# Performance work log

Measured on AMD Instinct MI355X. Metric: run time of the kernel, lower is better.

Reference implementation:

```python
import jax, jax.numpy as jnp
import numpy as np

D_MODEL = 1024
EXPAND = 2
D_INNER = EXPAND * D_MODEL          # 2048
HEADDIM = 64
NHEADS = D_INNER // HEADDIM         # 32
D_STATE = 128
NGROUPS = 1
D_CONV = 4
CONV_DIM = D_INNER + 2 * NGROUPS * D_STATE   # 2304
D_IN_PROJ = 2 * D_INNER + 2 * NGROUPS * D_STATE + NHEADS  # 4384
EPS = 1e-5


def setup_inputs() -> dict:
    key = jax.random.key(0)
    ks = jax.random.split(key, 12)
    x = jax.random.normal(ks[0], (2, 2048, D_MODEL), dtype=jnp.float32)
    in_proj_w = jax.random.normal(ks[1], (D_IN_PROJ, D_MODEL), dtype=jnp.float32) * 0.02
    conv_w = jax.random.normal(ks[2], (CONV_DIM, D_CONV), dtype=jnp.float32) * 0.2
    conv_b = jax.random.normal(ks[3], (CONV_DIM,), dtype=jnp.float32) * 0.02
    # dt_bias from inverse-softplus of dt ~ U(1e-3, 0.1)
    dt = jnp.exp(jax.random.uniform(ks[4], (NHEADS,)) * (np.log(0.1) - np.log(1e-3)) + np.log(1e-3))
    dt_bias = dt + jnp.log(-jnp.expm1(-dt))
    A_log = jnp.log(jax.random.uniform(ks[5], (NHEADS,), minval=1.0, maxval=16.0))
    D_skip = jnp.ones((NHEADS,), dtype=jnp.float32)
    norm_w = jnp.ones((D_INNER,), dtype=jnp.float32)
    out_w = jax.random.normal(ks[6], (D_MODEL, D_INNER), dtype=jnp.float32) * 0.02
    ln_g = jnp.ones((D_MODEL,), dtype=jnp.float32)
    ln_b = jnp.zeros((D_MODEL,), dtype=jnp.float32)
    return {"x": x, "in_proj_w": in_proj_w, "conv_w": conv_w, "conv_b": conv_b,
            "dt_bias": dt_bias, "A_log": A_log, "D_skip": D_skip, "norm_w": norm_w,
            "out_w": out_w, "ln_g": ln_g, "ln_b": ln_b}


def _depthwise_causal_conv(x, w, b):
    # x: (B, L, C); w: (C, K); causal depthwise conv (torch Conv1d groups=C, padding=K-1, truncated)
    K = w.shape[1]
    y = jax.lax.conv_general_dilated(
        x.transpose(0, 2, 1), w[:, None, :], (1,), [(K - 1, 0)],
        feature_group_count=w.shape[0], dimension_numbers=("NCH", "OIH", "NCH"))
    return y.transpose(0, 2, 1) + b


def _ssd_scan(xh, dt, A, Bm, Cm):
    # xh: (B,L,H,P), dt: (B,L,H), A: (H,), Bm/Cm: (B,L,N)  (ngroups=1)
    dA = jnp.exp(dt * A)  # (B,L,H)

    def step(h, inp):
        dA_t, dt_t, x_t, B_t, C_t = inp
        h = dA_t[..., None, None] * h + jnp.einsum("bh,bhp,bn->bhpn", dt_t, x_t, B_t)
        y = jnp.einsum("bhpn,bn->bhp", h, C_t)
        return h, y

    Bsz, L, H, P = xh.shape
    N = Bm.shape[-1]
    h0 = jnp.zeros((Bsz, H, P, N), dtype=xh.dtype)
    inputs = (dA.transpose(1, 0, 2), dt.transpose(1, 0, 2),
              xh.transpose(1, 0, 2, 3), Bm.transpose(1, 0, 2), Cm.transpose(1, 0, 2))
    _, ys = jax.lax.scan(step, h0, inputs)  # ys: (L,B,H,P)
    return ys.transpose(1, 0, 2, 3)


def reference(x, in_proj_w, conv_w, conv_b, dt_bias, A_log, D_skip, norm_w, out_w, ln_g, ln_b):
    B, L, D = x.shape
    residual = x  # D is a multiple of 8 -> pad branch is a no-op

    zxbcdt = jnp.einsum("bld,ed->ble", x, in_proj_w)  # (B,L,D_IN_PROJ)
    z = zxbcdt[..., :D_INNER]
    xBC = zxbcdt[..., D_INNER:D_INNER + CONV_DIM]
    dt = jax.nn.softplus(zxbcdt[..., D_INNER + CONV_DIM:] + dt_bias)  # (B,L,H)

    xBC = jax.nn.silu(_depthwise_causal_conv(xBC, conv_w, conv_b))
    xh = xBC[..., :D_INNER].reshape(B, L, NHEADS, HEADDIM)
    Bm = xBC[..., D_INNER:D_INNER + D_STATE]
    Cm = xBC[..., D_INNER + D_STATE:]

    A = -jnp.exp(A_log)  # (H,)
    y = _ssd_scan(xh, dt, A, Bm, Cm)          # (B,L,H,P)
    y = y + xh * D_skip[None, None, :, None]  # D skip connection
    y = y.reshape(B, L, D_INNER)

    # gated RMSNorm: normalize y * silu(z)
    y = y * jax.nn.silu(z)
    y = y * jax.lax.rsqrt(jnp.mean(y * y, axis=-1, keepdims=True) + EPS) * norm_w

    out = jnp.einsum("ble,de->bld", y, out_w)  # (B,L,D)

    # block LayerNorm + residual (dropout p=0 -> identity)
    mu = jnp.mean(out, axis=-1, keepdims=True)
    var = jnp.mean(jnp.square(out - mu), axis=-1, keepdims=True)
    out = (out - mu) * jax.lax.rsqrt(var + EPS) * ln_g + ln_b
    return out + residual
```

## Files before the change

### kernel.cpp

```cpp
#include <hip/hip_runtime.h>
#include <math.h>

#define D_MODEL   1024
#define D_INNER   2048
#define HEADDIM   64
#define NHEADS    32
#define D_STATE   128
#define D_CONV    4
#define CONV_DIM  2304
#define D_IN_PROJ 4384
#define NPAD      4480
#define LSEQ      2048
#define BATCH     2
#define NROWS     4096
#define NC        32

typedef __attribute__((ext_vector_type(8))) short short8_t;
typedef __attribute__((ext_vector_type(4))) float f32x4;

#define MFMA16(a, b, c) __builtin_amdgcn_mfma_f32_16x16x32_bf16(a, b, c, 0, 0, 0)

#define GLDS(g, l) __builtin_amdgcn_global_load_lds( \
    (const __attribute__((address_space(1))) unsigned int*)(g), \
    (__attribute__((address_space(3))) unsigned int*)(l), 16, 0, 0)

__device__ __forceinline__ unsigned short f2bf(float f) {
  union { float f; unsigned int u; } v; v.f = f;
  unsigned int u = v.u + 0x7FFFu + ((v.u >> 16) & 1u);
  return (unsigned short)(u >> 16);
}
__device__ __forceinline__ float bf2f(unsigned short h) {
  union { unsigned int u; float f; } v; v.u = ((unsigned int)h) << 16;
  return v.f;
}

__device__ __forceinline__ short8_t lds_frag(const unsigned short* base, int row,
                                             int col, int rowlen) {
  int off = (row * rowlen + col) * 2;
  off ^= (row & 7) << 4;
  return *reinterpret_cast<const short8_t*>(
      reinterpret_cast<const char*>(base) + off);
}
__device__ __forceinline__ void lds_w32(unsigned short* base, int row, int col,
                                        int rowlen, unsigned int val) {
  int off = (row * rowlen + col) * 2;
  off ^= (row & 7) << 4;
  *reinterpret_cast<unsigned int*>(reinterpret_cast<char*>(base) + off) = val;
}
__device__ __forceinline__ void lds_w16(unsigned short* base, int row, int col,
                                        int rowlen, unsigned short val) {
  int off = (row * rowlen + col) * 2;
  off ^= (row & 7) << 4;
  *reinterpret_cast<unsigned short*>(reinterpret_cast<char*>(base) + off) = val;
}
__device__ __forceinline__ unsigned short lds_r16(const unsigned short* base,
                                                  int row, int col, int rowlen) {
  int off = (row * rowlen + col) * 2;
  off ^= (row & 7) << 4;
  return *reinterpret_cast<const unsigned short*>(
      reinterpret_cast<const char*>(base) + off);
}

__global__ __launch_bounds__(256) void gemm_bf16(
    const unsigned short* __restrict__ A, const unsigned short* __restrict__ B,
    float* __restrict__ C, int N, int K) {
  __shared__ unsigned short sA[128 * 64];
  __shared__ unsigned short sB[128 * 64];
  const int tid = threadIdx.x;
  const int row0 = blockIdx.y * 128;
  const int col0 = blockIdx.x * 128;
  const int l  = tid & 63;
  const int la = l & 15;
  const int lk = (l >> 4) * 8;
  const int w  = tid >> 6;
  const int wr = (w >> 1) * 64;
  const int wc = (w & 1) * 64;

  f32x4 acc[4][4];
  #pragma unroll
  for (int i = 0; i < 4; ++i)
    #pragma unroll
    for (int j = 0; j < 4; ++j) acc[i][j] = (f32x4){0.f, 0.f, 0.f, 0.f};

  for (int k0 = 0; k0 < K; k0 += 64) {
    __syncthreads();
    #pragma unroll
    for (int i = 0; i < 4; ++i) {
      int s = i * 256 + tid;
      int r = s >> 3;
      int j = s & 7;
      int jc = j ^ (r & 7);
      GLDS(&A[(size_t)(row0 + r) * K + k0 + jc * 8], &sA[s * 8]);
      GLDS(&B[(size_t)(col0 + r) * K + k0 + jc * 8], &sB[s * 8]);
    }
    __syncthreads();

    #pragma unroll
    for (int kk = 0; kk < 2; ++kk) {
      short8_t af[4], bfr[4];
      #pragma unroll
      for (int mi = 0; mi < 4; ++mi)
        af[mi] = lds_frag(sA, wr + mi * 16 + la, kk * 32 + lk, 64);
      #pragma unroll
      for (int ni = 0; ni < 4; ++ni)
        bfr[ni] = lds_frag(sB, wc + ni * 16 + la, kk * 32 + lk, 64);
      #pragma unroll
      for (int mi = 0; mi < 4; ++mi)
        #pragma unroll
        for (int ni = 0; ni < 4; ++ni)
          acc[mi][ni] = MFMA16(af[mi], bfr[ni], acc[mi][ni]);
    }
  }

  #pragma unroll
  for (int mi = 0; mi < 4; ++mi)
    #pragma unroll
    for (int ni = 0; ni < 4; ++ni)
      #pragma unroll
      for (int r = 0; r < 4; ++r) {
        int gm = row0 + wr + mi * 16 + (l >> 4) * 4 + r;
        int gn = col0 + wc + ni * 16 + la;
        if (gn < N) C[(size_t)gm * N + gn] = acc[mi][ni][r];
      }
}

__global__ __launch_bounds__(256) void cvt_bf16_kernel(
    const float* __restrict__ src, unsigned short* __restrict__ dst) {
  long i = (long)blockIdx.x * 256 + threadIdx.x;
  float4 a = *reinterpret_cast<const float4*>(&src[i * 8]);
  float4 b = *reinterpret_cast<const float4*>(&src[i * 8 + 4]);
  short8_t o;
  o[0] = (short)f2bf(a.x); o[1] = (short)f2bf(a.y);
  o[2] = (short)f2bf(a.z); o[3] = (short)f2bf(a.w);
  o[4] = (short)f2bf(b.x); o[5] = (short)f2bf(b.y);
  o[6] = (short)f2bf(b.z); o[7] = (short)f2bf(b.w);
  *reinterpret_cast<short8_t*>(&dst[i * 8]) = o;
}

__global__ __launch_bounds__(256) void cvt_w_kernel(
    const float* __restrict__ w, unsigned short* __restrict__ wbf) {
  long i = (long)blockIdx.x * 256 + threadIdx.x;
  int row = (int)(i >> 7);
  int c8  = (int)(i & 127) << 3;
  short8_t o = {0, 0, 0, 0, 0, 0, 0, 0};
  if (row < D_IN_PROJ) {
    float4 a = *reinterpret_cast<const float4*>(&w[(size_t)row * D_MODEL + c8]);
    float4 b = *reinterpret_cast<const float4*>(&w[(size_t)row * D_MODEL + c8 + 4]);
    o[0] = (short)f2bf(a.x); o[1] = (short)f2bf(a.y);
    o[2] = (short)f2bf(a.z); o[3] = (short)f2bf(a.w);
    o[4] = (short)f2bf(b.x); o[5] = (short)f2bf(b.y);
    o[6] = (short)f2bf(b.z); o[7] = (short)f2bf(b.w);
  }
  *reinterpret_cast<short8_t*>(&wbf[(size_t)row * D_MODEL + c8]) = o;
}

__global__ __launch_bounds__(256) void conv_silu_kernel(
    const float* __restrict__ zxbcdt, const float* __restrict__ conv_w,
    const float* __restrict__ conv_b, float* __restrict__ xconv) {
  const int c = blockIdx.x * 256 + threadIdx.x;
  const int l = blockIdx.y;
  const int b = blockIdx.z;
  const float* src = zxbcdt + ((size_t)b * LSEQ) * D_IN_PROJ + D_INNER + c;
  float w0 = conv_w[c * 4 + 0], w1 = conv_w[c * 4 + 1];
  float w2 = conv_w[c * 4 + 2], w3 = conv_w[c * 4 + 3];
  float acc = conv_b[c];
  if (l >= 3) acc = fmaf(w0, src[(size_t)(l - 3) * D_IN_PROJ], acc);
  if (l >= 2) acc = fmaf(w1, src[(size_t)(l - 2) * D_IN_PROJ], acc);
  if (l >= 1) acc = fmaf(w2, src[(size_t)(l - 1) * D_IN_PROJ], acc);
  acc = fmaf(w3, src[(size_t)l * D_IN_PROJ], acc);
  float s = acc / (1.f + expf(-acc));
  xconv[((size_t)b * LSEQ + l) * CONV_DIM + c] = s;
}

__global__ __launch_bounds__(256) void dt_kernel(
    const float* __restrict__ zxbcdt, const float* __restrict__ dt_bias,
    float* __restrict__ dt_out) {
  int idx = blockIdx.x * 256 + threadIdx.x;
  int h = idx & 31;
  int row = idx >> 5;
  float x = zxbcdt[(size_t)row * D_IN_PROJ + (D_INNER + CONV_DIM) + h] + dt_bias[h];
  float dt = (x > 20.f) ? x : log1pf(expf(x));
  dt_out[idx] = dt;
}

__global__ __launch_bounds__(256) void cumsum_kernel(
    const float* __restrict__ dt_s, const float* __restrict__ A_log,
    float* __restrict__ cumL) {
  int u = blockIdx.x * 4 + (threadIdx.x >> 6);
  int lane = threadIdx.x & 63;
  int h = u & 31;
  int bc = u >> 5;
  int row = bc * 64 + lane;
  float A = -expf(A_log[h]);
  float a = dt_s[(size_t)row * NHEADS + h] * A;
  #pragma unroll
  for (int off = 1; off < 64; off <<= 1) {
    float v = __shfl_up(a, off);
    if (lane >= off) a += v;
  }
  cumL[(size_t)u * 64 + lane] = a;
}

__global__ __launch_bounds__(256) void chunkstate_kernel(
    const float* __restrict__ xconv, const float* __restrict__ dt_s,
    const float* __restrict__ cumL, unsigned short* __restrict__ S) {
  const int bi = blockIdx.x;
  const int h  = bi & 31;
  const int bc = bi >> 5;
  const int row0 = bc * 64;
  const int tid = threadIdx.x;

  __shared__ unsigned short sBT[128 * 64];
  __shared__ unsigned short sXT[64 * 64];
  __shared__ float sw[64];

  if (tid < 64) {
    float L   = cumL[(size_t)bi * 64 + tid];
    float L63 = cumL[(size_t)bi * 64 + 63];
    sw[tid] = dt_s[(size_t)(row0 + tid) * NHEADS + h] * expf(L63 - L);
  }
  __syncthreads();

  #pragma unroll
  for (int i = 0; i < 16; ++i) {
    int idx = tid + i * 256;
    int s = idx >> 6, n2 = idx & 63;
    float2 v = *reinterpret_cast<const float2*>(
        &xconv[(size_t)(row0 + s) * CONV_DIM + D_INNER + n2 * 2]);
    lds_w16(sBT, n2 * 2 + 0, s, 64, f2bf(v.x));
    lds_w16(sBT, n2 * 2 + 1, s, 64, f2bf(v.y));
  }
  #pragma unroll
  for (int i = 0; i < 16; ++i) {
    int idx = tid + i * 256;
    int s = idx >> 6, p = idx & 63;
    float xv = xconv[(size_t)(row0 + s) * CONV_DIM + h * HEADDIM + p];
    lds_w16(sXT, p, s, 64, f2bf(xv * sw[s]));
  }
  __syncthreads();

  const int w  = tid >> 6;
  const int l  = tid & 63;
  const int la = l & 15;
  const int lk = (l >> 4) * 8;

  f32x4 acc[8];
  #pragma unroll
  for (int i = 0; i < 8; ++i) acc[i] = (f32x4){0.f, 0.f, 0.f, 0.f};

  #pragma unroll
  for (int ks = 0; ks < 2; ++ks) {
    short8_t a = lds_frag(sXT, 16 * w + la, ks * 32 + lk, 64);
    #pragma unroll
    for (int ni = 0; ni < 8; ++ni) {
      short8_t b = lds_frag(sBT, ni * 16 + la, ks * 32 + lk, 64);
      acc[ni] = MFMA16(a, b, acc[ni]);
    }
  }

  unsigned short* dst = S + (size_t)bi * (HEADDIM * D_STATE);
  #pragma unroll
  for (int ni = 0; ni < 8; ++ni)
    #pragma unroll
    for (int r = 0; r < 4; ++r) {
      int p = 16 * w + (l >> 4) * 4 + r;
      int n = ni * 16 + la;
      dst[p * D_STATE + n] = f2bf(acc[ni][r]);
    }
}

__global__ __launch_bounds__(256) void hscan_kernel(
    unsigned short* __restrict__ S, const float* __restrict__ cumL) {
  const int g  = blockIdx.x;
  const int bh = g >> 5;
  const int b  = bh >> 5;
  const int h  = bh & 31;
  const int e  = (g & 31) * 256 + threadIdx.x;

  float H = 0.f;
  #pragma unroll 4
  for (int c = 0; c < NC; ++c) {
    size_t u = (size_t)((b * NC + c) * NHEADS + h);
    float dA = expf(cumL[u * 64 + 63]);
    unsigned short sv = S[u * (HEADDIM * D_STATE) + e];
    S[u * (HEADDIM * D_STATE) + e] = f2bf(H);
    H = dA * H + bf2f(sv);
  }
}

__global__ __launch_bounds__(256) void chunk_kernel(
    const float* __restrict__ xconv, const float* __restrict__ dt_s,
    const float* __restrict__ cumL, const unsigned short* __restrict__ Hprev,
    const float* __restrict__ D_skip, unsigned short* __restrict__ y) {
  const int bi = blockIdx.x;
  const int h  = bi & 31;
  const int bc = bi >> 5;
  const int row0 = bc * 64;
  const int tid = threadIdx.x;

  __shared__ unsigned short sC[64 * 128];
  __shared__ unsigned short sB[64 * 128];
  __shared__ unsigned short sXT[64 * 64];
  __shared__ unsigned short sP[64 * 64];
  __shared__ float sL[64], sdt[64], seL[64];

  if (tid < 64) {
    float L = cumL[(size_t)bi * 64 + tid];
    sL[tid]  = L;
    seL[tid] = expf(L);
    sdt[tid] = dt_s[(size_t)(row0 + tid) * NHEADS + h];
  }

  #pragma unroll
  for (int i = 0; i < 16; ++i) {
    int idx = tid + i * 256;
    int r = idx >> 6, q = idx & 63;
    float4 v = *reinterpret_cast<const float4*>(
        &xconv[(size_t)(row0 + r) * CONV_DIM + D_INNER + q * 4]);
    unsigned int u0 = (unsigned int)f2bf(v.x) | ((unsigned int)f2bf(v.y) << 16);
    unsigned int u1 = (unsigned int)f2bf(v.z) | ((unsigned int)f2bf(v.w) << 16);
    if (q < 32) {
      lds_w32(sB, r, q * 4 + 0, 128, u0);
      lds_w32(sB, r, q * 4 + 2, 128, u1);
    } else {
      lds_w32(sC, r, (q - 32) * 4 + 0, 128, u0);
      lds_w32(sC, r, (q - 32) * 4 + 2, 128, u1);
    }
  }
  #pragma unroll
  for (int i = 0; i < 16; ++i) {
    int idx = tid + i * 256;
    int s = idx >> 6, p = idx & 63;
    float xv = xconv[(size_t)(row0 + s) * CONV_DIM + h * HEADDIM + p];
    lds_w16(sXT, p, s, 64, f2bf(xv));
  }
  __syncthreads();

  const int w  = tid >> 6;
  const int l  = tid & 63;
  const int la = l & 15;
  const int lk = (l >> 4) * 8;
  const int t0 = 16 * w;

  f32x4 g[4];
  #pragma unroll
  for (int i = 0; i < 4; ++i) g[i] = (f32x4){0.f, 0.f, 0.f, 0.f};
  #pragma unroll
  for (int ks = 0; ks < 4; ++ks) {
    short8_t a = lds_frag(sC, t0 + la, ks * 32 + lk, 128);
    #pragma unroll
    for (int si = 0; si < 4; ++si) {
      short8_t b = lds_frag(sB, si * 16 + la, ks * 32 + lk, 128);
      g[si] = MFMA16(a, b, g[si]);
    }
  }
  #pragma unroll
  for (int si = 0; si < 4; ++si)
    #pragma unroll
    for (int r = 0; r < 4; ++r) {
      int t = t0 + (l >> 4) * 4 + r;
      int s = si * 16 + la;
      float m = 0.f;
      if (s <= t) m = expf(sL[t] - sL[s]) * sdt[s] * g[si][r];
      lds_w16(sP, t, s, 64, f2bf(m));
    }
  __syncthreads();

  f32x4 o[4];
  #pragma unroll
  for (int i = 0; i < 4; ++i) o[i] = (f32x4){0.f, 0.f, 0.f, 0.f};

  const unsigned short* hb = Hprev + (size_t)bi * (HEADDIM * D_STATE);
  #pragma unroll
  for (int ks = 0; ks < 4; ++ks) {
    short8_t a = lds_frag(sC, t0 + la, ks * 32 + lk, 128);
    #pragma unroll
    for (int si = 0; si < 4; ++si) {
      int p = si * 16 + la;
      short8_t b = *reinterpret_cast<const short8_t*>(
          &hb[p * D_STATE + ks * 32 + lk]);
      o[si] = MFMA16(a, b, o[si]);
    }
  }
  #pragma unroll
  for (int si = 0; si < 4; ++si)
    #pragma unroll
    for (int r = 0; r < 4; ++r) {
      int t = t0 + (l >> 4) * 4 + r;
      o[si][r] *= seL[t];
    }
  #pragma unroll
  for (int ks = 0; ks < 2; ++ks) {
    short8_t a = lds_frag(sP, t0 + la, ks * 32 + lk, 64);
    #pragma unroll
    for (int si = 0; si < 4; ++si) {
      short8_t b = lds_frag(sXT, si * 16 + la, ks * 32 + lk, 64);
      o[si] = MFMA16(a, b, o[si]);
    }
  }
  const float Dh = D_skip[h];
  #pragma unroll
  for (int si = 0; si < 4; ++si)
    #pragma unroll
    for (int r = 0; r < 4; ++r) {
      int t = t0 + (l >> 4) * 4 + r;
      int p = si * 16 + la;
      float xv = bf2f(lds_r16(sXT, p, t, 64));
      y[(size_t)(row0 + t) * D_INNER + h * HEADDIM + p] = f2bf(o[si][r] + Dh * xv);
    }
}

__global__ __launch_bounds__(256) void gate_rms_kernel(
    unsigned short* __restrict__ y, const float* __restrict__ zxbcdt,
    const float* __restrict__ norm_w) {
  const int row = blockIdx.x;
  const int tid = threadIdx.x;
  float v[8];
  float acc = 0.f;
  #pragma unroll
  for (int i = 0; i < 8; ++i) {
    int d = i * 256 + tid;
    float ys = bf2f(y[(size_t)row * D_INNER + d]);
    float z  = zxbcdt[(size_t)row * D_IN_PROJ + d];
    float gz = z / (1.f + expf(-z));
    float val = ys * gz;
    v[i] = val;
    acc = fmaf(val, val, acc);
  }
  #pragma unroll
  for (int off = 32; off; off >>= 1) acc += __shfl_xor(acc, off);
  __shared__ float wsum[4];
  if ((tid & 63) == 0) wsum[tid >> 6] = acc;
  __syncthreads();
  float total = wsum[0] + wsum[1] + wsum[2] + wsum[3];
  float scale = rsqrtf(total / (float)D_INNER + 1e-5f);
  #pragma unroll
  for (int i = 0; i < 8; ++i) {
    int d = i * 256 + tid;
    y[(size_t)row * D_INNER + d] = f2bf(v[i] * scale * norm_w[d]);
  }
}

__global__ __launch_bounds__(256) void ln_kernel(
    const float* __restrict__ o, const float* __restrict__ x,
    const float* __restrict__ lng, const float* __restrict__ lnb,
    float* __restrict__ out) {
  const int row = blockIdx.x;
  const int tid = threadIdx.x;
  float v[4];
  float s = 0.f, s2 = 0.f;
  #pragma unroll
  for (int i = 0; i < 4; ++i) {
    int d = i * 256 + tid;
    float t = o[(size_t)row * D_MODEL + d];
    v[i] = t;
    s += t;
    s2 = fmaf(t, t, s2);
  }
  #pragma unroll
  for (int off = 32; off; off >>= 1) {
    s  += __shfl_xor(s, off);
    s2 += __shfl_xor(s2, off);
  }
  __shared__ float sa[4], sb[4];
  if ((tid & 63) == 0) { sa[tid >> 6] = s; sb[tid >> 6] = s2; }
  __syncthreads();
  s  = sa[0] + sa[1] + sa[2] + sa[3];
  s2 = sb[0] + sb[1] + sb[2] + sb[3];
  float mu  = s / (float)D_MODEL;
  float var = s2 / (float)D_MODEL - mu * mu;
  float inv = rsqrtf(var + 1e-5f);
  #pragma unroll
  for (int i = 0; i < 4; ++i) {
    int d = i * 256 + tid;
    out[(size_t)row * D_MODEL + d] =
        (v[i] - mu) * inv * lng[d] + lnb[d] + x[(size_t)row * D_MODEL + d];
  }
}

extern "C" void kernel_launch(void* const* d_in, const int* in_sizes, int n_in,
                              void* d_out, int out_size, void* d_ws, size_t ws_size,
                              hipStream_t stream) {
  const float* x         = (const float*)d_in[0];
  const float* in_proj_w = (const float*)d_in[1];
  const float* conv_w    = (const float*)d_in[2];
  const float* conv_b    = (const float*)d_in[3];
  const float* dt_bias   = (const float*)d_in[4];
  const float* A_log     = (const float*)d_in[5];
  const float* D_skip    = (const float*)d_in[6];
  const float* norm_w    = (const float*)d_in[7];
  const float* out_w     = (const float*)d_in[8];
  const float* ln_g      = (const float*)d_in[9];
  const float* ln_b      = (const float*)d_in[10];
  float* out = (float*)d_out;

  float* ws      = (float*)d_ws;
  float* zxbcdt  = ws;
  float* xconv   = zxbcdt + (size_t)NROWS * D_IN_PROJ;
  float* dt_s    = xconv + (size_t)NROWS * CONV_DIM;
  float* cumL    = dt_s + (size_t)NROWS * NHEADS;
  unsigned short* schp = (unsigned short*)(cumL + (size_t)BATCH * NC * NHEADS * 64);
  unsigned short* ybuf = schp + (size_t)BATCH * NC * NHEADS * HEADDIM * D_STATE;
  unsigned short* xbf  = ybuf + (size_t)NROWS * D_INNER;
  unsigned short* wbf  = xbf + (size_t)NROWS * D_MODEL;
  unsigned short* owbf = wbf + (size_t)NPAD * D_MODEL;
  float* outpre  = zxbcdt;

  cvt_bf16_kernel<<<dim3(NROWS * D_MODEL / 8 / 256), dim3(256), 0, stream>>>(
      x, xbf);
  cvt_w_kernel<<<dim3(NPAD * 128 / 256), dim3(256), 0, stream>>>(
      in_proj_w, wbf);
  cvt_bf16_kernel<<<dim3(D_MODEL * D_INNER / 8 / 256), dim3(256), 0, stream>>>(
      out_w, owbf);

  gemm_bf16<<<dim3(NPAD / 128, NROWS / 128), dim3(256), 0, stream>>>(
      xbf, wbf, zxbcdt, D_IN_PROJ, D_MODEL);

  conv_silu_kernel<<<dim3(CONV_DIM / 256, LSEQ, BATCH), dim3(256), 0, stream>>>(
      zxbcdt, conv_w, conv_b, xconv);

  dt_kernel<<<dim3(NROWS * NHEADS / 256), dim3(256), 0, stream>>>(
      zxbcdt, dt_bias, dt_s);

  cumsum_kernel<<<dim3(BATCH * NC * NHEADS / 4), dim3(256), 0, stream>>>(
      dt_s, A_log, cumL);

  chunkstate_kernel<<<dim3(BATCH * NC * NHEADS), dim3(256), 0, stream>>>(
      xconv, dt_s, cumL, schp);

  hscan_kernel<<<dim3(BATCH * NHEADS * 32), dim3(256), 0, stream>>>(
      schp, cumL);

  chunk_kernel<<<dim3(BATCH * NC * NHEADS), dim3(256), 0, stream>>>(
      xconv, dt_s, cumL, schp, D_skip, ybuf);

  gate_rms_kernel<<<dim3(NROWS), dim3(256), 0, stream>>>(
      ybuf, zxbcdt, norm_w);

  gemm_bf16<<<dim3(D_MODEL / 128, NROWS / 128), dim3(256), 0, stream>>>(
      ybuf, owbf, outpre, D_MODEL, D_INNER);

  ln_kernel<<<dim3(NROWS), dim3(256), 0, stream>>>(
      outpre, x, ln_g, ln_b, out);
}
```

Measured before the change: 351.9 us.

## Store in_proj output and conv activations in bf16, swizzle GEMM block order

The in_proj GEMM now writes its output as bf16, plus a separate fp32 buffer for the dt columns. The conv output is also kept in bf16, which roughly halves intermediate traffic for the conv, chunk, chunkstate and gate kernels. The conv kernel processes 128 timesteps per thread with a sliding window instead of one per block. Gate RMS uses vectorized 16-byte loads and stores. GEMM blocks are remapped with an XCD-style swizzle for L2 locality. The extra bf16 rounding of z, x, B and C adds precision loss, and the output alias now reuses the bf16 region as an fp32 outpre buffer.

```diff
diff --git a/kernel.cpp b/kernel.cpp
--- a/kernel.cpp
+++ b/kernel.cpp
@@ -61,14 +61,19 @@
       reinterpret_cast<const char*>(base) + off);
 }
 
+template <int MODE>
 __global__ __launch_bounds__(256) void gemm_bf16(
     const unsigned short* __restrict__ A, const unsigned short* __restrict__ B,
-    float* __restrict__ C, int N, int K) {
+    void* __restrict__ Cout, float* __restrict__ dtraw, int N, int K) {
   __shared__ unsigned short sA[128 * 64];
   __shared__ unsigned short sB[128 * 64];
   const int tid = threadIdx.x;
-  const int row0 = blockIdx.y * 128;
-  const int col0 = blockIdx.x * 128;
+  const int lin = blockIdx.y * gridDim.x + blockIdx.x;
+  const int cpx = (gridDim.x * gridDim.y) >> 3;
+  const int swz = (lin & 7) * cpx + (lin >> 3);
+  const int row0 = (swz / gridDim.x) * 128;
+  const int col0 = (swz % gridDim.x) * 128;
+
   const int l  = tid & 63;
   const int la = l & 15;
   const int lk = (l >> 4) * 8;
@@ -120,7 +125,14 @@
       for (int r = 0; r < 4; ++r) {
         int gm = row0 + wr + mi * 16 + (l >> 4) * 4 + r;
         int gn = col0 + wc + ni * 16 + la;
-        if (gn < N) C[(size_t)gm * N + gn] = acc[mi][ni][r];
+        if (gn < N) {
+          if constexpr (MODE == 0) {
+            ((float*)Cout)[(size_t)gm * N + gn] = acc[mi][ni][r];
+          } else {
+            ((unsigned short*)Cout)[(size_t)gm * N + gn] = f2bf(acc[mi][ni][r]);
+            if (gn >= N - 32) dtraw[(size_t)gm * 32 + (gn - (N - 32))] = acc[mi][ni][r];
+          }
+        }
       }
 }
 
@@ -155,30 +167,35 @@
 }
 
 __global__ __launch_bounds__(256) void conv_silu_kernel(
-    const float* __restrict__ zxbcdt, const float* __restrict__ conv_w,
-    const float* __restrict__ conv_b, float* __restrict__ xconv) {
-  const int c = blockIdx.x * 256 + threadIdx.x;
-  const int l = blockIdx.y;
-  const int b = blockIdx.z;
-  const float* src = zxbcdt + ((size_t)b * LSEQ) * D_IN_PROJ + D_INNER + c;
-  float w0 = conv_w[c * 4 + 0], w1 = conv_w[c * 4 + 1];
-  float w2 = conv_w[c * 4 + 2], w3 = conv_w[c * 4 + 3];
-  float acc = conv_b[c];
-  if (l >= 3) acc = fmaf(w0, src[(size_t)(l - 3) * D_IN_PROJ], acc);
-  if (l >= 2) acc = fmaf(w1, src[(size_t)(l - 2) * D_IN_PROJ], acc);
-  if (l >= 1) acc = fmaf(w2, src[(size_t)(l - 1) * D_IN_PROJ], acc);
-  acc = fmaf(w3, src[(size_t)l * D_IN_PROJ], acc);
-  float s = acc / (1.f + expf(-acc));
-  xconv[((size_t)b * LSEQ + l) * CONV_DIM + c] = s;
+    const unsigned short* __restrict__ zxb, const float* __restrict__ conv_w,
+    const float* __restrict__ conv_b, unsigned short* __restrict__ xconv) {
+  const int c  = blockIdx.x * 256 + threadIdx.x;
+  const int l0 = blockIdx.y * 128;
+  const int b  = blockIdx.z;
+  const unsigned short* src = zxb + ((size_t)b * LSEQ) * D_IN_PROJ + D_INNER + c;
+  const float w0 = conv_w[c * 4 + 0], w1 = conv_w[c * 4 + 1];
+  const float w2 = conv_w[c * 4 + 2], w3 = conv_w[c * 4 + 3];
+  const float bia = conv_b[c];
+  float x0 = (l0 >= 3) ? bf2f(src[(size_t)(l0 - 3) * D_IN_PROJ]) : 0.f;
+  float x1 = (l0 >= 2) ? bf2f(src[(size_t)(l0 - 2) * D_IN_PROJ]) : 0.f;
+  float x2 = (l0 >= 1) ? bf2f(src[(size_t)(l0 - 1) * D_IN_PROJ]) : 0.f;
+  unsigned short* dst = xconv + ((size_t)(b * LSEQ + l0)) * CONV_DIM + c;
+  #pragma unroll 4
+  for (int i = 0; i < 128; ++i) {
+    float x3 = bf2f(src[(size_t)(l0 + i) * D_IN_PROJ]);
+    float acc = fmaf(w3, x3, fmaf(w2, x2, fmaf(w1, x1, fmaf(w0, x0, bia))));
+    float s = acc / (1.f + expf(-acc));
+    dst[(size_t)i * CONV_DIM] = f2bf(s);
+    x0 = x1; x1 = x2; x2 = x3;
+  }
 }
 
 __global__ __launch_bounds__(256) void dt_kernel(
-    const float* __restrict__ zxbcdt, const float* __restrict__ dt_bias,
+    const float* __restrict__ dtraw, const float* __restrict__ dt_bias,
     float* __restrict__ dt_out) {
   int idx = blockIdx.x * 256 + threadIdx.x;
   int h = idx & 31;
-  int row = idx >> 5;
-  float x = zxbcdt[(size_t)row * D_IN_PROJ + (D_INNER + CONV_DIM) + h] + dt_bias[h];
+  float x = dtraw[idx] + dt_bias[h];
   float dt = (x > 20.f) ? x : log1pf(expf(x));
   dt_out[idx] = dt;
 }
@@ -202,7 +219,7 @@
 }
 
 __global__ __launch_bounds__(256) void chunkstate_kernel(
-    const float* __restrict__ xconv, const float* __restrict__ dt_s,
+    const unsigned short* __restrict__ xconv, const float* __restrict__ dt_s,
     const float* __restrict__ cumL, unsigned short* __restrict__ S) {
   const int bi = blockIdx.x;
   const int h  = bi & 31;
@@ -225,16 +242,16 @@
   for (int i = 0; i < 16; ++i) {
     int idx = tid + i * 256;
     int s = idx >> 6, n2 = idx & 63;
-    float2 v = *reinterpret_cast<const float2*>(
+    unsigned int v = *reinterpret_cast<const unsigned int*>(
         &xconv[(size_t)(row0 + s) * CONV_DIM + D_INNER + n2 * 2]);
-    lds_w16(sBT, n2 * 2 + 0, s, 64, f2bf(v.x));
-    lds_w16(sBT, n2 * 2 + 1, s, 64, f2bf(v.y));
+    lds_w16(sBT, n2 * 2 + 0, s, 64, (unsigned short)v);
+    lds_w16(sBT, n2 * 2 + 1, s, 64, (unsigned short)(v >> 16));
   }
   #pragma unroll
   for (int i = 0; i < 16; ++i) {
     int idx = tid + i * 256;
     int s = idx >> 6, p = idx & 63;
-    float xv = xconv[(size_t)(row0 + s) * CONV_DIM + h * HEADDIM + p];
+    float xv = bf2f(xconv[(size_t)(row0 + s) * CONV_DIM + h * HEADDIM + p]);
     lds_w16(sXT, p, s, 64, f2bf(xv * sw[s]));
   }
   __syncthreads();
@@ -289,7 +306,7 @@
 }
 
 __global__ __launch_bounds__(256) void chunk_kernel(
-    const float* __restrict__ xconv, const float* __restrict__ dt_s,
+    const unsigned short* __restrict__ xconv, const float* __restrict__ dt_s,
     const float* __restrict__ cumL, const unsigned short* __restrict__ Hprev,
     const float* __restrict__ D_skip, unsigned short* __restrict__ y) {
   const int bi = blockIdx.x;
@@ -312,27 +329,32 @@
   }
 
   #pragma unroll
-  for (int i = 0; i < 16; ++i) {
+  for (int i = 0; i < 8; ++i) {
     int idx = tid + i * 256;
-    int r = idx >> 6, q = idx & 63;
-    float4 v = *reinterpret_cast<const float4*>(
-        &xconv[(size_t)(row0 + r) * CONV_DIM + D_INNER + q * 4]);
-    unsigned int u0 = (unsigned int)f2bf(v.x) | ((unsigned int)f2bf(v.y) << 16);
-    unsigned int u1 = (unsigned int)f2bf(v.z) | ((unsigned int)f2bf(v.w) << 16);
-    if (q < 32) {
-      lds_w32(sB, r, q * 4 + 0, 128, u0);
-      lds_w32(sB, r, q * 4 + 2, 128, u1);
-    } else {
-      lds_w32(sC, r, (q - 32) * 4 + 0, 128, u0);
-      lds_w32(sC, r, (q - 32) * 4 + 2, 128, u1);
-    }
+    int r = idx >> 5, q = idx & 31;
+    short8_t v = *reinterpret_cast<const short8_t*>(
+        &xconv[(size_t)(row0 + r) * CONV_DIM + D_INNER + q * 8]);
+    unsigned int u0 = (unsigned int)(unsigned short)v[0] |
+                      ((unsigned int)(unsigned short)v[1] << 16);
+    unsigned int u1 = (unsigned int)(unsigned short)v[2] |
+                      ((unsigned int)(unsigned short)v[3] << 16);
+    unsigned int u2 = (unsigned int)(unsigned short)v[4] |
+                      ((unsigned int)(unsigned short)v[5] << 16);
+    unsigned int u3 = (unsigned int)(unsigned short)v[6] |
+                      ((unsigned int)(unsigned short)v[7] << 16);
+    unsigned short* dstb = (q < 16) ? sB : sC;
+    int cq = (q & 15) * 8;
+    lds_w32(dstb, r, cq + 0, 128, u0);
+    lds_w32(dstb, r, cq + 2, 128, u1);
+    lds_w32(dstb, r, cq + 4, 128, u2);
+    lds_w32(dstb, r, cq + 6, 128, u3);
   }
   #pragma unroll
   for (int i = 0; i < 16; ++i) {
     int idx = tid + i * 256;
     int s = idx >> 6, p = idx & 63;
-    float xv = xconv[(size_t)(row0 + s) * CONV_DIM + h * HEADDIM + p];
-    lds_w16(sXT, p, s, 64, f2bf(xv));
+    lds_w16(sXT, p, s, 64,
+            xconv[(size_t)(row0 + s) * CONV_DIM + h * HEADDIM + p]);
   }
   __syncthreads();
 
@@ -411,17 +433,20 @@
 }
 
 __global__ __launch_bounds__(256) void gate_rms_kernel(
-    unsigned short* __restrict__ y, const float* __restrict__ zxbcdt,
+    unsigned short* __restrict__ y, const unsigned short* __restrict__ zxb,
     const float* __restrict__ norm_w) {
   const int row = blockIdx.x;
   const int tid = threadIdx.x;
+  short8_t zv = *reinterpret_cast<const short8_t*>(
+      &zxb[(size_t)row * D_IN_PROJ + tid * 8]);
+  short8_t yv = *reinterpret_cast<short8_t*>(
+      &y[(size_t)row * D_INNER + tid * 8]);
   float v[8];
   float acc = 0.f;
   #pragma unroll
   for (int i = 0; i < 8; ++i) {
-    int d = i * 256 + tid;
-    float ys = bf2f(y[(size_t)row * D_INNER + d]);
-    float z  = zxbcdt[(size_t)row * D_IN_PROJ + d];
+    float z  = bf2f((unsigned short)zv[i]);
+    float ys = bf2f((unsigned short)yv[i]);
     float gz = z / (1.f + expf(-z));
     float val = ys * gz;
     v[i] = val;
@@ -434,11 +459,11 @@
   __syncthreads();
   float total = wsum[0] + wsum[1] + wsum[2] + wsum[3];
   float scale = rsqrtf(total / (float)D_INNER + 1e-5f);
-  #pragma unroll
-  for (int i = 0; i < 8; ++i) {
-    int d = i * 256 + tid;
-    y[(size_t)row * D_INNER + d] = f2bf(v[i] * scale * norm_w[d]);
-  }
+  short8_t o;
+  #pragma unroll
+  for (int i = 0; i < 8; ++i)
+    o[i] = (short)f2bf(v[i] * scale * norm_w[tid * 8 + i]);
+  *reinterpret_cast<short8_t*>(&y[(size_t)row * D_INNER + tid * 8]) = o;
 }
 
 __global__ __launch_bounds__(256) void ln_kernel(
@@ -494,17 +519,19 @@
   const float* ln_b      = (const float*)d_in[10];
   float* out = (float*)d_out;
 
-  float* ws      = (float*)d_ws;
-  float* zxbcdt  = ws;
-  float* xconv   = zxbcdt + (size_t)NROWS * D_IN_PROJ;
-  float* dt_s    = xconv + (size_t)NROWS * CONV_DIM;
-  float* cumL    = dt_s + (size_t)NROWS * NHEADS;
-  unsigned short* schp = (unsigned short*)(cumL + (size_t)BATCH * NC * NHEADS * 64);
-  unsigned short* ybuf = schp + (size_t)BATCH * NC * NHEADS * HEADDIM * D_STATE;
-  unsigned short* xbf  = ybuf + (size_t)NROWS * D_INNER;
-  unsigned short* wbf  = xbf + (size_t)NROWS * D_MODEL;
-  unsigned short* owbf = wbf + (size_t)NPAD * D_MODEL;
-  float* outpre  = zxbcdt;
+  char* ws = (char*)d_ws;
+  unsigned short* zxb   = (unsigned short*)ws;
+  float* outpre         = (float*)ws;
+  char* p = ws + (size_t)NROWS * D_IN_PROJ * 2;
+  float* dtraw = (float*)p;            p += (size_t)NROWS * 32 * 4;
+  float* dt_s  = (float*)p;            p += (size_t)NROWS * 32 * 4;
+  float* cumL  = (float*)p;            p += (size_t)BATCH * NC * NHEADS * 64 * 4;
+  unsigned short* xconv = (unsigned short*)p;  p += (size_t)NROWS * CONV_DIM * 2;
+  unsigned short* schp  = (unsigned short*)p;  p += (size_t)BATCH * NC * NHEADS * HEADDIM * D_STATE * 2;
+  unsigned short* ybuf  = (unsigned short*)p;  p += (size_t)NROWS * D_INNER * 2;
+  unsigned short* xbf   = (unsigned short*)p;  p += (size_t)NROWS * D_MODEL * 2;
+  unsigned short* wbf   = (unsigned short*)p;  p += (size_t)NPAD * D_MODEL * 2;
+  unsigned short* owbf  = (unsigned short*)p;
 
   cvt_bf16_kernel<<<dim3(NROWS * D_MODEL / 8 / 256), dim3(256), 0, stream>>>(
       x, xbf);
@@ -513,14 +540,14 @@
   cvt_bf16_kernel<<<dim3(D_MODEL * D_INNER / 8 / 256), dim3(256), 0, stream>>>(
       out_w, owbf);
 
-  gemm_bf16<<<dim3(NPAD / 128, NROWS / 128), dim3(256), 0, stream>>>(
-      xbf, wbf, zxbcdt, D_IN_PROJ, D_MODEL);
-
-  conv_silu_kernel<<<dim3(CONV_DIM / 256, LSEQ, BATCH), dim3(256), 0, stream>>>(
-      zxbcdt, conv_w, conv_b, xconv);
+  gemm_bf16<1><<<dim3(NPAD / 128, NROWS / 128), dim3(256), 0, stream>>>(
+      xbf, wbf, zxb, dtraw, D_IN_PROJ, D_MODEL);
+
+  conv_silu_kernel<<<dim3(CONV_DIM / 256, LSEQ / 128, BATCH), dim3(256), 0, stream>>>(
+      zxb, conv_w, conv_b, xconv);
 
   dt_kernel<<<dim3(NROWS * NHEADS / 256), dim3(256), 0, stream>>>(
-      zxbcdt, dt_bias, dt_s);
+      dtraw, dt_bias, dt_s);
 
   cumsum_kernel<<<dim3(BATCH * NC * NHEADS / 4), dim3(256), 0, stream>>>(
       dt_s, A_log, cumL);
@@ -535,10 +562,10 @@
       xconv, dt_s, cumL, schp, D_skip, ybuf);
 
   gate_rms_kernel<<<dim3(NROWS), dim3(256), 0, stream>>>(
-      ybuf, zxbcdt, norm_w);
-
-  gemm_bf16<<<dim3(D_MODEL / 128, NROWS / 128), dim3(256), 0, stream>>>(
-      ybuf, owbf, outpre, D_MODEL, D_INNER);
+      ybuf, zxb, norm_w);
+
+  gemm_bf16<0><<<dim3(D_MODEL / 128, NROWS / 128), dim3(256), 0, stream>>>(
+      ybuf, owbf, outpre, nullptr, D_MODEL, D_INNER);
 
   ln_kernel<<<dim3(NROWS), dim3(256), 0, stream>>>(
       outpre, x, ln_g, ln_b, out);
```

Measured after the change: 322.3 us. 8.4% less time.
